# Kernel optimization log

Measured on AMD Instinct MI355X. Metric: run time of the kernel, lower is better.

Reference implementation:

```python
import jax, jax.numpy as jnp
import numpy as np

B, S, D_IN, D_OUT = 4, 2048, 4096, 16384


def setup_inputs() -> dict:
    key = jax.random.key(0)
    k1, k2, k3, k4 = jax.random.split(key, 4)
    x = jax.random.normal(k1, (B, S, D_IN), dtype=jnp.float32)
    # per-channel symmetric int8 weights, [out_features, in_features]
    weight_int8 = jax.random.randint(k2, (D_OUT, D_IN), -128, 128, dtype=jnp.int32).astype(jnp.int8)
    # per-channel weight scales (positive, realistic magnitude)
    weight_scale = jax.random.uniform(k3, (D_OUT,), dtype=jnp.float32) * 0.01 + 1e-4
    # static per-tensor activation scale (calibrated constant)
    act_scale = jnp.float32(0.02)
    bias = jax.random.normal(k4, (D_OUT,), dtype=jnp.float32) * 0.1
    return {"x": x, "weight_int8": weight_int8, "weight_scale": weight_scale,
            "act_scale": act_scale, "bias": bias}


def reference(x, weight_int8, weight_scale, act_scale, bias):
    orig_shape = x.shape
    orig_dtype = x.dtype
    x2d = x.reshape(-1, orig_shape[-1])  # [M, D_in]
    # static per-tensor symmetric activation quantization
    x_int8 = jnp.clip(jnp.round(x2d.astype(jnp.float32) / act_scale), -128, 127).astype(jnp.int8)
    y_int32 = jnp.matmul(x_int8, weight_int8.T, preferred_element_type=jnp.int32)  # [M, D_out]
    output_scale = (act_scale * weight_scale).astype(jnp.float32)  # [D_out]
    y = y_int32.astype(jnp.float32) * output_scale[None, :] + bias.astype(jnp.float32)[None, :]
    return y.reshape(*orig_shape[:-1], y.shape[-1]).astype(orig_dtype)
```

## Files before the change

### kernel.cpp

```cpp
#include <hip/hip_runtime.h>
#include <stdint.h>

#define GAS __attribute__((address_space(1)))
#define LAS __attribute__((address_space(3)))

typedef int v4i __attribute__((ext_vector_type(4)));

constexpr int Mdim = 8192;
constexpr int Ndim = 16384;
constexpr int Kdim = 4096;

__device__ __forceinline__ int pack4i8(int a, int b, int c, int d) {
    return (a & 255) | ((b & 255) << 8) | ((c & 255) << 16) | ((d & 255) << 24);
}

__device__ __forceinline__ int qz(float v, float inv) {
    return (int)fminf(fmaxf(rintf(v * inv), -128.0f), 127.0f);
}

__global__ void k_quant_x(const float* __restrict__ x, const float* __restrict__ asc,
                          int8_t* __restrict__ xq) {
    const int i = blockIdx.x * blockDim.x + threadIdx.x;
    const float inv = 1.0f / *asc;
    const float4* xv = (const float4*)x + (size_t)i * 4;
    float4 f0 = xv[0], f1 = xv[1], f2 = xv[2], f3 = xv[3];
    int4 o;
    o.x = pack4i8(qz(f0.x, inv), qz(f0.y, inv), qz(f0.z, inv), qz(f0.w, inv));
    o.y = pack4i8(qz(f1.x, inv), qz(f1.y, inv), qz(f1.z, inv), qz(f1.w, inv));
    o.z = pack4i8(qz(f2.x, inv), qz(f2.y, inv), qz(f2.z, inv), qz(f2.w, inv));
    o.w = pack4i8(qz(f3.x, inv), qz(f3.y, inv), qz(f3.z, inv), qz(f3.w, inv));
    ((int4*)xq)[i] = o;
}

__global__ void k_conv_w(const int* __restrict__ w, int8_t* __restrict__ wq) {
    const int i = blockIdx.x * blockDim.x + threadIdx.x;
    const int4* wv = (const int4*)w + (size_t)i * 4;
    int4 a = wv[0], b = wv[1], c = wv[2], d = wv[3];
    int4 o;
    o.x = pack4i8(a.x, a.y, a.z, a.w);
    o.y = pack4i8(b.x, b.y, b.z, b.w);
    o.z = pack4i8(c.x, c.y, c.z, c.w);
    o.w = pack4i8(d.x, d.y, d.z, d.w);
    ((int4*)wq)[i] = o;
}

constexpr int NSTEP = Kdim / 64;

__global__ __launch_bounds__(512, 2)
void k_gemm256(const int8_t* __restrict__ Aq, const int8_t* __restrict__ Bq,
               const float* __restrict__ wscale, const float* __restrict__ asc,
               const float* __restrict__ bias, float* __restrict__ out) {
    __shared__ __align__(16) int8_t lds[131072];
    const int tid = threadIdx.x, lane = tid & 63, w = tid >> 6;
    const int wm = w >> 2, wn = w & 3;
    const int lrow = lane & 15, kgrp = lane >> 4;

    const int bid = blockIdx.x;
    const int swz = ((bid & 7) << 8) | (bid >> 3);
    const int mt = swz & 31, nt = swz >> 5;
    const int m0 = mt << 8, n0 = nt << 8;

    int8_t* const A_lds = lds;
    int8_t* const B_lds = lds + 65536;

    const int srow = (w << 4) + (lane >> 2);
    const int scol = (((lane & 3) ^ ((lane >> 3) & 3)) << 4);
    const int8_t* gAu0 = Aq + (size_t)(m0 + srow) * Kdim + scol;
    const int8_t* gAu1 = Aq + (size_t)(m0 + 128 + srow) * Kdim + scol;
    const int8_t* gBu0 = Bq + (size_t)(n0 + srow) * Kdim + scol;
    const int8_t* gBu1 = Bq + (size_t)(n0 + 128 + srow) * Kdim + scol;
    const int dstoff = w << 10;

    auto stageB2 = [&](int s2) {
        int8_t* base = B_lds + ((s2 & 3) << 14) + dstoff;
        __builtin_amdgcn_global_load_lds((const GAS void*)(gBu0 + s2 * 64), (LAS void*)base, 16, 0, 0);
        __builtin_amdgcn_global_load_lds((const GAS void*)(gBu1 + s2 * 64), (LAS void*)(base + 8192), 16, 0, 0);
    };
    auto stageA2 = [&](int s2) {
        int8_t* base = A_lds + ((s2 & 3) << 14) + dstoff;
        __builtin_amdgcn_global_load_lds((const GAS void*)(gAu0 + s2 * 64), (LAS void*)base, 16, 0, 0);
        __builtin_amdgcn_global_load_lds((const GAS void*)(gAu1 + s2 * 64), (LAS void*)(base + 8192), 16, 0, 0);
    };

    const int kc = (kgrp ^ ((lrow >> 1) & 3)) << 4;
    const int arowb = (((wm << 7) + lrow) << 6) + kc;
    const int browb = (((wn << 6) + lrow) << 6) + kc;

    v4i acc[8][4];
#pragma unroll
    for (int i = 0; i < 8; ++i)
#pragma unroll
        for (int j = 0; j < 4; ++j) acc[i][j] = (v4i){0, 0, 0, 0};

    stageB2(0); stageA2(0); stageB2(1); stageA2(1);
    asm volatile("s_waitcnt vmcnt(4)" ::: "memory");
    __builtin_amdgcn_s_barrier();

    v4i a[4], b[4];
    for (int s = 0; s < NSTEP; ++s) {
        const int8_t* As_ = A_lds + ((s & 3) << 14);
        const int8_t* Bs_ = B_lds + ((s & 3) << 14);
        const bool st = s < NSTEP - 2;
#pragma unroll
        for (int f = 0; f < 4; ++f)
            b[f] = *(const v4i*)(Bs_ + browb + f * 1024);
#pragma unroll
        for (int f = 0; f < 4; ++f)
            a[f] = *(const v4i*)(As_ + arowb + f * 1024);
        if (st) stageB2(s + 2);
        __builtin_amdgcn_s_barrier();
        asm volatile("s_waitcnt lgkmcnt(0)" ::: "memory");
        __builtin_amdgcn_sched_barrier(0);
        __builtin_amdgcn_s_setprio(1);
#pragma unroll
        for (int fi = 0; fi < 4; ++fi)
#pragma unroll
            for (int fj = 0; fj < 4; ++fj)
                acc[fi][fj] = __builtin_amdgcn_mfma_i32_16x16x64_i8(a[fi], b[fj], acc[fi][fj], 0, 0, 0);
        __builtin_amdgcn_s_setprio(0);
        __builtin_amdgcn_s_barrier();
#pragma unroll
        for (int f = 0; f < 4; ++f)
            a[f] = *(const v4i*)(As_ + arowb + 4096 + f * 1024);
        if (st) stageA2(s + 2);
        if (st)                    asm volatile("s_waitcnt vmcnt(4)" ::: "memory");
        else if (s == NSTEP - 2)   asm volatile("s_waitcnt vmcnt(0)" ::: "memory");
        __builtin_amdgcn_s_barrier();
        asm volatile("s_waitcnt lgkmcnt(0)" ::: "memory");
        __builtin_amdgcn_sched_barrier(0);
        __builtin_amdgcn_s_setprio(1);
#pragma unroll
        for (int fi = 0; fi < 4; ++fi)
#pragma unroll
            for (int fj = 0; fj < 4; ++fj)
                acc[4 + fi][fj] = __builtin_amdgcn_mfma_i32_16x16x64_i8(a[fi], b[fj], acc[4 + fi][fj], 0, 0, 0);
        __builtin_amdgcn_s_setprio(0);
        __builtin_amdgcn_s_barrier();
    }

    const float ascale = *asc;
#pragma unroll
    for (int fj = 0; fj < 4; ++fj) {
        const int col = n0 + (wn << 6) + fj * 16 + lrow;
        const float sc = ascale * wscale[col];
        const float bb = bias[col];
#pragma unroll
        for (int mi = 0; mi < 8; ++mi) {
            const int r0 = m0 + (wm << 7) + mi * 16 + (kgrp << 2);
            float* o = out + (size_t)r0 * Ndim + col;
#pragma unroll
            for (int q = 0; q < 4; ++q)
                o[(size_t)q * Ndim] = (float)acc[mi][fj][q] * sc + bb;
        }
    }
}

template <bool AQ, bool BQ>
__global__ __launch_bounds__(256)
void k_gemm(const int8_t* __restrict__ Aq, const float* __restrict__ Xf,
            const int8_t* __restrict__ Bq, const int* __restrict__ W32,
            const float* __restrict__ wscale, const float* __restrict__ asc,
            const float* __restrict__ bias, float* __restrict__ out) {
    constexpr int BM = 128, BN = 128, BK = 64;
    constexpr int KT = Kdim / BK;
    __shared__ __align__(16) int8_t As[2][BM * BK];
    __shared__ __align__(16) int8_t Bs[2][BN * BK];

    const int tid  = threadIdx.x;
    const int lane = tid & 63;
    const int wid  = tid >> 6;
    const int wm = wid >> 1, wn = wid & 1;
    const int lrow = lane & 15, kgrp = lane >> 4;

    const int cpx = gridDim.x >> 3;
    const int swz = ((int)blockIdx.x & 7) * cpx + ((int)blockIdx.x >> 3);
    const int mt = swz & (Mdim / BM - 1);
    const int nt = swz / (Mdim / BM);
    const int m0 = mt * BM, n0 = nt * BN;

    const float ascale = *asc;
    const float inv = 1.0f / ascale;

    v4i acc[4][4];
#pragma unroll
    for (int i = 0; i < 4; ++i)
#pragma unroll
        for (int j = 0; j < 4; ++j) acc[i][j] = (v4i){0, 0, 0, 0};

    auto stage = [&](int buf, int kt) {
        const int k0 = kt * BK;
        if constexpr (AQ) {
            int8_t* ldsp = &As[buf][wid << 10];
            const int8_t* g = Aq + (size_t)(m0 + (tid >> 2)) * Kdim + k0 + ((tid & 3) << 4);
            __builtin_amdgcn_global_load_lds((const GAS void*)g, (LAS void*)ldsp, 16, 0, 0);
            __builtin_amdgcn_global_load_lds((const GAS void*)(g + (size_t)64 * Kdim),
                                             (LAS void*)(ldsp + 4096), 16, 0, 0);
        } else {
            const int row = tid >> 1, cb = (tid & 1) << 5;
            const float4* src = (const float4*)(Xf + (size_t)(m0 + row) * Kdim + k0 + cb);
            int t[8];
#pragma unroll
            for (int j = 0; j < 8; ++j) {
                float4 f = src[j];
                t[j] = pack4i8(qz(f.x, inv), qz(f.y, inv), qz(f.z, inv), qz(f.w, inv));
            }
            int4* dst = (int4*)&As[buf][row * BK + cb];
            dst[0] = make_int4(t[0], t[1], t[2], t[3]);
            dst[1] = make_int4(t[4], t[5], t[6], t[7]);
        }
        if constexpr (BQ) {
            int8_t* ldsp = &Bs[buf][wid << 10];
            const int8_t* g = Bq + (size_t)(n0 + (tid >> 2)) * Kdim + k0 + ((tid & 3) << 4);
            __builtin_amdgcn_global_load_lds((const GAS void*)g, (LAS void*)ldsp, 16, 0, 0);
            __builtin_amdgcn_global_load_lds((const GAS void*)(g + (size_t)64 * Kdim),
                                             (LAS void*)(ldsp + 4096), 16, 0, 0);
        } else {
            const int row = tid >> 1, cb = (tid & 1) << 5;
            const int4* src = (const int4*)(W32 + (size_t)(n0 + row) * Kdim + k0 + cb);
            int t[8];
#pragma unroll
            for (int j = 0; j < 8; ++j) {
                int4 vv = src[j];
                t[j] = pack4i8(vv.x, vv.y, vv.z, vv.w);
            }
            int4* dst = (int4*)&Bs[buf][row * BK + cb];
            dst[0] = make_int4(t[0], t[1], t[2], t[3]);
            dst[1] = make_int4(t[4], t[5], t[6], t[7]);
        }
    };

    stage(0, 0);
    for (int kt = 0; kt < KT; ++kt) {
        const int cur = kt & 1;
        __syncthreads();
        if (kt + 1 < KT) stage(cur ^ 1, kt + 1);

        v4i a[4], b[4];
        const int koff = kgrp << 4;
#pragma unroll
        for (int i = 0; i < 4; ++i) {
            a[i] = *(const v4i*)&As[cur][(wm * 64 + i * 16 + lrow) * BK + koff];
            b[i] = *(const v4i*)&Bs[cur][(wn * 64 + i * 16 + lrow) * BK + koff];
        }
#pragma unroll
        for (int i = 0; i < 4; ++i)
#pragma unroll
            for (int j = 0; j < 4; ++j)
                acc[i][j] = __builtin_amdgcn_mfma_i32_16x16x64_i8(a[i], b[j], acc[i][j], 0, 0, 0);
    }

#pragma unroll
    for (int j = 0; j < 4; ++j) {
        const int col = n0 + wn * 64 + j * 16 + lrow;
        const float sc = ascale * wscale[col];
        const float bb = bias[col];
#pragma unroll
        for (int i = 0; i < 4; ++i) {
            const int r0 = m0 + wm * 64 + i * 16 + (kgrp << 2);
            float* o = out + (size_t)r0 * Ndim + col;
#pragma unroll
            for (int r = 0; r < 4; ++r)
                o[(size_t)r * Ndim] = (float)acc[i][j][r] * sc + bb;
        }
    }
}

extern "C" void kernel_launch(void* const* d_in, const int* in_sizes, int n_in,
                              void* d_out, int out_size, void* d_ws, size_t ws_size,
                              hipStream_t stream) {
    const float* x      = (const float*)d_in[0];
    const int*   w32    = (const int*)d_in[1];
    const float* wscale = (const float*)d_in[2];
    const float* asc    = (const float*)d_in[3];
    const float* bias   = (const float*)d_in[4];
    float* out = (float*)d_out;

    const size_t nx = (size_t)Mdim * Kdim;
    const size_t nw = (size_t)Ndim * Kdim;
    int8_t* xq = (int8_t*)d_ws;
    int8_t* wq = xq + nx;

    const bool haveX = ws_size >= nx;
    const bool haveW = ws_size >= nx + nw;

    if (haveX) k_quant_x<<<(int)(nx / 16 / 256), 256, 0, stream>>>(x, asc, xq);
    if (haveW) k_conv_w<<<(int)(nw / 16 / 256), 256, 0, stream>>>(w32, wq);

    if (haveW) {
        dim3 grid((Mdim / 256) * (Ndim / 256));
        k_gemm256<<<grid, 512, 0, stream>>>(xq, wq, wscale, asc, bias, out);
    } else if (haveX) {
        dim3 grid((Mdim / 128) * (Ndim / 128));
        k_gemm<true, false><<<grid, 256, 0, stream>>>(xq, x, wq, w32, wscale, asc, bias, out);
    } else {
        dim3 grid((Mdim / 128) * (Ndim / 128));
        k_gemm<false, false><<<grid, 256, 0, stream>>>(xq, x, wq, w32, wscale, asc, bias, out);
    }
}
```

Measured before the change: 823.9 us.

## Register double-buffer LDS fragments and prefetch three k-stages ahead

Restructures the GEMM main loop so that LDS fragments for the next k-step are read into a second register set while MFMAs run on the current set. This replaces the split half-A/half-B phases, which used four barriers per step, with one barrier per step. Global-to-LDS staging now runs three stages ahead across a 4-slot ring instead of two. The cost is roughly doubled fragment registers (two sets of 8 A and 4 B v4i), which may push VGPR pressure at 512 threads with 2 blocks per CU, and a tighter slot-reuse ordering that could race.

Result: slower. 923.9 us (+12.1%).

```diff
diff --git a/kernel.cpp b/kernel.cpp
--- a/kernel.cpp
+++ b/kernel.cpp
@@ -60,82 +60,79 @@
     const int mt = swz & 31, nt = swz >> 5;
     const int m0 = mt << 8, n0 = nt << 8;
 
-    int8_t* const A_lds = lds;
-    int8_t* const B_lds = lds + 65536;
-
     const int srow = (w << 4) + (lane >> 2);
     const int scol = (((lane & 3) ^ ((lane >> 3) & 3)) << 4);
-    const int8_t* gAu0 = Aq + (size_t)(m0 + srow) * Kdim + scol;
-    const int8_t* gAu1 = Aq + (size_t)(m0 + 128 + srow) * Kdim + scol;
-    const int8_t* gBu0 = Bq + (size_t)(n0 + srow) * Kdim + scol;
-    const int8_t* gBu1 = Bq + (size_t)(n0 + 128 + srow) * Kdim + scol;
+    const int8_t* pA0 = Aq + (size_t)(m0 + srow) * Kdim + scol;
+    const int8_t* pA1 = pA0 + (size_t)128 * Kdim;
+    const int8_t* pB0 = Bq + (size_t)(n0 + srow) * Kdim + scol;
+    const int8_t* pB1 = pB0 + (size_t)128 * Kdim;
     const int dstoff = w << 10;
 
-    auto stageB2 = [&](int s2) {
-        int8_t* base = B_lds + ((s2 & 3) << 14) + dstoff;
-        __builtin_amdgcn_global_load_lds((const GAS void*)(gBu0 + s2 * 64), (LAS void*)base, 16, 0, 0);
-        __builtin_amdgcn_global_load_lds((const GAS void*)(gBu1 + s2 * 64), (LAS void*)(base + 8192), 16, 0, 0);
-    };
-    auto stageA2 = [&](int s2) {
-        int8_t* base = A_lds + ((s2 & 3) << 14) + dstoff;
-        __builtin_amdgcn_global_load_lds((const GAS void*)(gAu0 + s2 * 64), (LAS void*)base, 16, 0, 0);
-        __builtin_amdgcn_global_load_lds((const GAS void*)(gAu1 + s2 * 64), (LAS void*)(base + 8192), 16, 0, 0);
+    auto stage = [&](int slot, int kb) {
+        int8_t* ba = lds + (slot << 14) + dstoff;
+        int8_t* bb = lds + 65536 + (slot << 14) + dstoff;
+        __builtin_amdgcn_global_load_lds((const GAS void*)(pB0 + kb), (LAS void*)bb, 16, 0, 0);
+        __builtin_amdgcn_global_load_lds((const GAS void*)(pB1 + kb), (LAS void*)(bb + 8192), 16, 0, 0);
+        __builtin_amdgcn_global_load_lds((const GAS void*)(pA0 + kb), (LAS void*)ba, 16, 0, 0);
+        __builtin_amdgcn_global_load_lds((const GAS void*)(pA1 + kb), (LAS void*)(ba + 8192), 16, 0, 0);
     };
 
     const int kc = (kgrp ^ ((lrow >> 1) & 3)) << 4;
     const int arowb = (((wm << 7) + lrow) << 6) + kc;
     const int browb = (((wn << 6) + lrow) << 6) + kc;
 
-    v4i acc[8][4];
-#pragma unroll
-    for (int i = 0; i < 8; ++i)
-#pragma unroll
-        for (int j = 0; j < 4; ++j) acc[i][j] = (v4i){0, 0, 0, 0};
-
-    stageB2(0); stageA2(0); stageB2(1); stageA2(1);
-    asm volatile("s_waitcnt vmcnt(4)" ::: "memory");
-    __builtin_amdgcn_s_barrier();
-
-    v4i a[4], b[4];
-    for (int s = 0; s < NSTEP; ++s) {
-        const int8_t* As_ = A_lds + ((s & 3) << 14);
-        const int8_t* Bs_ = B_lds + ((s & 3) << 14);
-        const bool st = s < NSTEP - 2;
+    auto readfr = [&](int slot, v4i* a, v4i* b) {
+        const int8_t* As_ = lds + (slot << 14);
+        const int8_t* Bs_ = lds + 65536 + (slot << 14);
 #pragma unroll
         for (int f = 0; f < 4; ++f)
             b[f] = *(const v4i*)(Bs_ + browb + f * 1024);
 #pragma unroll
-        for (int f = 0; f < 4; ++f)
+        for (int f = 0; f < 8; ++f)
             a[f] = *(const v4i*)(As_ + arowb + f * 1024);
-        if (st) stageB2(s + 2);
-        __builtin_amdgcn_s_barrier();
-        asm volatile("s_waitcnt lgkmcnt(0)" ::: "memory");
-        __builtin_amdgcn_sched_barrier(0);
+    };
+
+    v4i acc[8][4];
+#pragma unroll
+    for (int i = 0; i < 8; ++i)
+#pragma unroll
+        for (int j = 0; j < 4; ++j) acc[i][j] = (v4i){0, 0, 0, 0};
+
+    auto domfma = [&](v4i* a, v4i* b) {
         __builtin_amdgcn_s_setprio(1);
 #pragma unroll
-        for (int fi = 0; fi < 4; ++fi)
+        for (int fi = 0; fi < 8; ++fi)
 #pragma unroll
             for (int fj = 0; fj < 4; ++fj)
                 acc[fi][fj] = __builtin_amdgcn_mfma_i32_16x16x64_i8(a[fi], b[fj], acc[fi][fj], 0, 0, 0);
         __builtin_amdgcn_s_setprio(0);
-        __builtin_amdgcn_s_barrier();
-#pragma unroll
-        for (int f = 0; f < 4; ++f)
-            a[f] = *(const v4i*)(As_ + arowb + 4096 + f * 1024);
-        if (st) stageA2(s + 2);
-        if (st)                    asm volatile("s_waitcnt vmcnt(4)" ::: "memory");
-        else if (s == NSTEP - 2)   asm volatile("s_waitcnt vmcnt(0)" ::: "memory");
-        __builtin_amdgcn_s_barrier();
-        asm volatile("s_waitcnt lgkmcnt(0)" ::: "memory");
-        __builtin_amdgcn_sched_barrier(0);
-        __builtin_amdgcn_s_setprio(1);
-#pragma unroll
-        for (int fi = 0; fi < 4; ++fi)
-#pragma unroll
-            for (int fj = 0; fj < 4; ++fj)
-                acc[4 + fi][fj] = __builtin_amdgcn_mfma_i32_16x16x64_i8(a[fi], b[fj], acc[4 + fi][fj], 0, 0, 0);
-        __builtin_amdgcn_s_setprio(0);
-        __builtin_amdgcn_s_barrier();
+    };
+
+    v4i aP[8], bP[4], aQ[8], bQ[4];
+
+    stage(0, 0); stage(1, 64); stage(2, 128);
+    asm volatile("s_waitcnt vmcnt(8)" ::: "memory");
+    __builtin_amdgcn_s_barrier();
+    readfr(0, aP, bP);
+
+    int kb = 192;
+    for (int s = 0; s < NSTEP; s += 2) {
+        if (s < NSTEP - 1) {
+            if (s == NSTEP - 2) asm volatile("s_waitcnt vmcnt(0)" ::: "memory");
+            else                asm volatile("s_waitcnt vmcnt(4)" ::: "memory");
+            __builtin_amdgcn_s_barrier();
+            readfr((s + 1) & 3, aQ, bQ);
+            if (s < NSTEP - 3) { stage((s + 3) & 3, kb); kb += 64; }
+        }
+        domfma(aP, bP);
+        const int t = s + 1;
+        if (t < NSTEP - 1) {
+            asm volatile("s_waitcnt vmcnt(4)" ::: "memory");
+            __builtin_amdgcn_s_barrier();
+            readfr((t + 1) & 3, aP, bP);
+            if (t < NSTEP - 3) { stage((t + 3) & 3, kb); kb += 64; }
+        }
+        domfma(aQ, bQ);
     }
 
     const float ascale = *asc;
```

## Replace 256x256 GEMM tile with 256x128 tile and double-buffered single-phase loop

Applied to the files above, without the earlier changes.

The int8 GEMM moves from a 512-thread, 256x256 tile with a four-slot LDS ring and two half-step MFMA phases to a 256-thread, 256x128 tile. It uses two 24KB LDS buffers, so LDS per block falls from 128KB to 48KB, and each wave does 8x4 MFMAs per K step. The aim is more resident blocks and fewer barriers per step. In exchange, arithmetic intensity per block drops (more global traffic for A), and each step waits with vmcnt(0), leaving less prefetch depth.

New measurement: 936.4 us. +13.7%, slower.

```diff
diff --git a/kernel.cpp b/kernel.cpp
--- a/kernel.cpp
+++ b/kernel.cpp
@@ -46,40 +46,43 @@
 
 constexpr int NSTEP = Kdim / 64;
 
-__global__ __launch_bounds__(512, 2)
-void k_gemm256(const int8_t* __restrict__ Aq, const int8_t* __restrict__ Bq,
+__global__ __launch_bounds__(256, 2)
+void k_gemm_pc(const int8_t* __restrict__ Aq, const int8_t* __restrict__ Bq,
                const float* __restrict__ wscale, const float* __restrict__ asc,
                const float* __restrict__ bias, float* __restrict__ out) {
-    __shared__ __align__(16) int8_t lds[131072];
+    __shared__ __align__(16) int8_t lds[49152];
     const int tid = threadIdx.x, lane = tid & 63, w = tid >> 6;
-    const int wm = w >> 2, wn = w & 3;
+    const int wm = w >> 1, wn = w & 1;
     const int lrow = lane & 15, kgrp = lane >> 4;
 
     const int bid = blockIdx.x;
-    const int swz = ((bid & 7) << 8) | (bid >> 3);
+    const int swz = ((bid & 7) << 9) | (bid >> 3);
     const int mt = swz & 31, nt = swz >> 5;
-    const int m0 = mt << 8, n0 = nt << 8;
-
-    int8_t* const A_lds = lds;
-    int8_t* const B_lds = lds + 65536;
+    const int m0 = mt << 8, n0 = nt << 7;
 
     const int srow = (w << 4) + (lane >> 2);
     const int scol = (((lane & 3) ^ ((lane >> 3) & 3)) << 4);
-    const int8_t* gAu0 = Aq + (size_t)(m0 + srow) * Kdim + scol;
-    const int8_t* gAu1 = Aq + (size_t)(m0 + 128 + srow) * Kdim + scol;
-    const int8_t* gBu0 = Bq + (size_t)(n0 + srow) * Kdim + scol;
-    const int8_t* gBu1 = Bq + (size_t)(n0 + 128 + srow) * Kdim + scol;
+    const int8_t* gA[4];
+    const int8_t* gB[2];
+#pragma unroll
+    for (int u = 0; u < 4; ++u)
+        gA[u] = Aq + (size_t)(m0 + u * 64 + srow) * Kdim + scol;
+#pragma unroll
+    for (int u = 0; u < 2; ++u)
+        gB[u] = Bq + (size_t)(n0 + u * 64 + srow) * Kdim + scol;
     const int dstoff = w << 10;
 
-    auto stageB2 = [&](int s2) {
-        int8_t* base = B_lds + ((s2 & 3) << 14) + dstoff;
-        __builtin_amdgcn_global_load_lds((const GAS void*)(gBu0 + s2 * 64), (LAS void*)base, 16, 0, 0);
-        __builtin_amdgcn_global_load_lds((const GAS void*)(gBu1 + s2 * 64), (LAS void*)(base + 8192), 16, 0, 0);
-    };
-    auto stageA2 = [&](int s2) {
-        int8_t* base = A_lds + ((s2 & 3) << 14) + dstoff;
-        __builtin_amdgcn_global_load_lds((const GAS void*)(gAu0 + s2 * 64), (LAS void*)base, 16, 0, 0);
-        __builtin_amdgcn_global_load_lds((const GAS void*)(gAu1 + s2 * 64), (LAS void*)(base + 8192), 16, 0, 0);
+    auto stage = [&](int slot, int kb) {
+        int8_t* ba = lds + slot * 24576 + dstoff;
+        int8_t* bb = ba + 16384;
+#pragma unroll
+        for (int u = 0; u < 2; ++u)
+            __builtin_amdgcn_global_load_lds((const GAS void*)(gB[u] + kb),
+                                             (LAS void*)(bb + u * 4096), 16, 0, 0);
+#pragma unroll
+        for (int u = 0; u < 4; ++u)
+            __builtin_amdgcn_global_load_lds((const GAS void*)(gA[u] + kb),
+                                             (LAS void*)(ba + u * 4096), 16, 0, 0);
     };
 
     const int kc = (kgrp ^ ((lrow >> 1) & 3)) << 4;
@@ -92,50 +95,32 @@
 #pragma unroll
         for (int j = 0; j < 4; ++j) acc[i][j] = (v4i){0, 0, 0, 0};
 
-    stageB2(0); stageA2(0); stageB2(1); stageA2(1);
-    asm volatile("s_waitcnt vmcnt(4)" ::: "memory");
-    __builtin_amdgcn_s_barrier();
-
-    v4i a[4], b[4];
+    v4i a[8], b[4];
+
+    stage(0, 0);
+    int kb = 64;
     for (int s = 0; s < NSTEP; ++s) {
-        const int8_t* As_ = A_lds + ((s & 3) << 14);
-        const int8_t* Bs_ = B_lds + ((s & 3) << 14);
-        const bool st = s < NSTEP - 2;
+        asm volatile("s_waitcnt vmcnt(0)" ::: "memory");
+        __builtin_amdgcn_s_barrier();
+        __builtin_amdgcn_sched_barrier(0);
+        const int8_t* As_ = lds + (s & 1) * 24576;
+        const int8_t* Bs_ = As_ + 16384;
 #pragma unroll
         for (int f = 0; f < 4; ++f)
             b[f] = *(const v4i*)(Bs_ + browb + f * 1024);
 #pragma unroll
-        for (int f = 0; f < 4; ++f)
+        for (int f = 0; f < 8; ++f)
             a[f] = *(const v4i*)(As_ + arowb + f * 1024);
-        if (st) stageB2(s + 2);
-        __builtin_amdgcn_s_barrier();
+        if (s < NSTEP - 1) { stage((s + 1) & 1, kb); kb += 64; }
         asm volatile("s_waitcnt lgkmcnt(0)" ::: "memory");
         __builtin_amdgcn_sched_barrier(0);
         __builtin_amdgcn_s_setprio(1);
 #pragma unroll
-        for (int fi = 0; fi < 4; ++fi)
+        for (int fi = 0; fi < 8; ++fi)
 #pragma unroll
             for (int fj = 0; fj < 4; ++fj)
                 acc[fi][fj] = __builtin_amdgcn_mfma_i32_16x16x64_i8(a[fi], b[fj], acc[fi][fj], 0, 0, 0);
         __builtin_amdgcn_s_setprio(0);
-        __builtin_amdgcn_s_barrier();
-#pragma unroll
-        for (int f = 0; f < 4; ++f)
-            a[f] = *(const v4i*)(As_ + arowb + 4096 + f * 1024);
-        if (st) stageA2(s + 2);
-        if (st)                    asm volatile("s_waitcnt vmcnt(4)" ::: "memory");
-        else if (s == NSTEP - 2)   asm volatile("s_waitcnt vmcnt(0)" ::: "memory");
-        __builtin_amdgcn_s_barrier();
-        asm volatile("s_waitcnt lgkmcnt(0)" ::: "memory");
-        __builtin_amdgcn_sched_barrier(0);
-        __builtin_amdgcn_s_setprio(1);
-#pragma unroll
-        for (int fi = 0; fi < 4; ++fi)
-#pragma unroll
-            for (int fj = 0; fj < 4; ++fj)
-                acc[4 + fi][fj] = __builtin_amdgcn_mfma_i32_16x16x64_i8(a[fi], b[fj], acc[4 + fi][fj], 0, 0, 0);
-        __builtin_amdgcn_s_setprio(0);
-        __builtin_amdgcn_s_barrier();
     }
 
     const float ascale = *asc;
@@ -287,8 +272,8 @@
     if (haveW) k_conv_w<<<(int)(nw / 16 / 256), 256, 0, stream>>>(w32, wq);
 
     if (haveW) {
-        dim3 grid((Mdim / 256) * (Ndim / 256));
-        k_gemm256<<<grid, 512, 0, stream>>>(xq, wq, wscale, asc, bias, out);
+        dim3 grid((Mdim / 256) * (Ndim / 128));
+        k_gemm_pc<<<grid, 256, 0, stream>>>(xq, wq, wscale, asc, bias, out);
     } else if (haveX) {
         dim3 grid((Mdim / 128) * (Ndim / 128));
         k_gemm<true, false><<<grid, 256, 0, stream>>>(xq, x, wq, w32, wscale, asc, bias, out);
```
